# Kernel tuning notes

Measured on AMD Instinct MI355X. Metric: run time of the kernel, lower is better.

## Reference

```python
import jax, jax.numpy as jnp
import numpy as np

N_NODES = 50000
N_EDGES = 800000
D_IN = 96
D_OUT = 96
K_ORDER = 3


def setup_inputs() -> dict:
    key = jax.random.key(0)
    k1, k2, k3, k4, k5 = jax.random.split(key, 5)
    rows = jax.random.randint(k1, (N_EDGES,), 0, N_NODES, dtype=jnp.int64 if jax.config.jax_enable_x64 else jnp.int32)
    cols = jax.random.randint(k2, (N_EDGES,), 0, N_NODES, dtype=jnp.int64 if jax.config.jax_enable_x64 else jnp.int32)
    vals = jax.random.uniform(k3, (N_EDGES,), dtype=jnp.float32) * (1.0 / 16.0)  # ~sym-normalized weights
    H = jax.random.normal(k4, (N_NODES, D_IN), dtype=jnp.float32)
    W = jax.random.normal(k5, (D_IN, D_OUT), dtype=jnp.float32) * (1.0 / np.sqrt(D_IN))
    bias = jnp.zeros((D_OUT,), dtype=jnp.float32)
    return {"rows": rows, "cols": cols, "vals": vals, "H": H, "W": W, "bias": bias}


def reference(rows, cols, vals, H, W, bias):
    n = H.shape[0]

    def spmm(X):  # L @ X via gather-multiply-scatter over COO edges
        return jax.ops.segment_sum(vals[:, None] * X[cols], rows, num_segments=n)

    def ln_mm(X):  # (2L - I) @ X
        return 2.0 * spmm(X) - X

    # k = 0 term: T_0 = H
    H_out = H @ W
    # k = 1 term: T_1 = (2L - I) H  (differentiable, as in torch code)
    T_prev = H
    T_curr = ln_mm(H)
    H_out = H_out + T_curr @ W
    # k >= 2: recurrence computed under no_grad in the original -> stop_gradient
    for _ in range(2, K_ORDER + 1):
        T_next = jax.lax.stop_gradient(2.0 * ln_mm(T_curr) - T_prev)
        H_out = H_out + T_next @ W
        T_prev, T_curr = T_curr, T_next
    return H_out + bias
```

## Files before the change

### kernel.cpp

```cpp
#include <hip/hip_runtime.h>
#include <hip/hip_fp16.h>

#define NN 50000
#define NE 800000
#define D  96
#define NB_SCAN 196
#define N4 (NN * D / 4)
#define CB4 ((N4 + 255) / 256)
#define WFRAG_BLKS 5
#define EMAX (NE + 8 * NN)
#define EZ4  (EMAX / 4)
#define EZB  ((EZ4 + 255) / 256)

typedef unsigned int   uint32;
typedef unsigned short uint16;
typedef short  v8s __attribute__((ext_vector_type(8)));
typedef float  v4f __attribute__((ext_vector_type(4)));
typedef unsigned int v2u __attribute__((ext_vector_type(2)));
typedef unsigned int v4u __attribute__((ext_vector_type(4)));
typedef float v2f __attribute__((ext_vector_type(2)));

__device__ inline uint16 f32_to_bf16(float f) {
    uint32 u = __float_as_uint(f);
    u += 0x7FFF + ((u >> 16) & 1);
    return (uint16)(u >> 16);
}

__device__ inline void u2f(v2u u, float& a, float& b, float& c, float& d) {
    a = __uint_as_float(u.x << 16);
    b = __uint_as_float(u.x & 0xFFFF0000u);
    c = __uint_as_float(u.y << 16);
    d = __uint_as_float(u.y & 0xFFFF0000u);
}

__device__ inline float f16_val(uint32 e) {
    __half_raw h; h.x = (uint16)(e >> 16);
    return __half2float(__half(h));
}

__global__ void prep(const float4* __restrict__ H, ushort4* __restrict__ Hb,
                     const float* __restrict__ W, uint16* __restrict__ Wfrag,
                     int* __restrict__ counts, v4u* __restrict__ edges4) {
    int b = blockIdx.x;
    int t = threadIdx.x;
    if (b < CB4) {
        int i = b * 256 + t;
        if (i < N4) {
            float4 v = H[i];
            ushort4 o;
            o.x = f32_to_bf16(v.x); o.y = f32_to_bf16(v.y);
            o.z = f32_to_bf16(v.z); o.w = f32_to_bf16(v.w);
            Hb[i] = o;
        }
    } else if (b < CB4 + NB_SCAN) {
        int i = (b - CB4) * 256 + t;
        if (i < NN) counts[i] = 0;
    } else if (b < CB4 + NB_SCAN + WFRAG_BLKS) {
        int idx = (b - CB4 - NB_SCAN) * 256 + t;
        if (idx < 18 * 64) {
            int bt = idx >> 6, lane = idx & 63;
            int nt = bt / 3, kc = bt % 3;
            int col = nt * 16 + (lane & 15);
            int kbase = kc * 32 + (lane >> 4) * 8;
            uint16 tmp[8];
            #pragma unroll
            for (int j = 0; j < 8; ++j) tmp[j] = f32_to_bf16(W[(kbase + j) * D + col]);
            uint32* dst = (uint32*)(Wfrag + ((size_t)bt * 64 + lane) * 8);
            const uint32* src = (const uint32*)tmp;
            #pragma unroll
            for (int j = 0; j < 4; ++j) dst[j] = src[j];
        }
    } else {
        int i = (b - CB4 - NB_SCAN - WFRAG_BLKS) * 256 + t;
        if (i < EZ4) edges4[i] = (v4u){0u, 0u, 0u, 0u};
    }
}

__global__ void hist_slots(const int* __restrict__ rows, int* __restrict__ counts,
                           int* __restrict__ slot) {
    int base = (blockIdx.x * blockDim.x + threadIdx.x) * 2;
    if (base < NE) {
        v2u rr = *(const v2u*)(rows + base);
        slot[base]     = atomicAdd(&counts[rr.x], 1);
        slot[base + 1] = atomicAdd(&counts[rr.y], 1);
    }
}

__global__ void scan_p1(const int* __restrict__ counts, int* __restrict__ partials) {
    __shared__ int red[256];
    int t = threadIdx.x;
    int i = blockIdx.x * 256 + t;
    red[t] = (i < NN) ? ((counts[i] + 7) & ~7) : 0;
    __syncthreads();
    for (int off = 128; off > 0; off >>= 1) {
        if (t < off) red[t] += red[t + off];
        __syncthreads();
    }
    if (t == 0) partials[blockIdx.x] = red[0];
}

__global__ void scan_p23(const int* __restrict__ counts, const int* __restrict__ partials,
                         int* __restrict__ row_ptr) {
    __shared__ int pp[256];
    __shared__ int sh[256];
    int t = threadIdx.x;
    pp[t] = (t < NB_SCAN) ? partials[t] : 0;
    __syncthreads();
    for (int off = 1; off < 256; off <<= 1) {
        int u = (t >= off) ? pp[t - off] : 0;
        __syncthreads();
        pp[t] += u;
        __syncthreads();
    }
    int blk_off = (blockIdx.x == 0) ? 0 : pp[blockIdx.x - 1];
    int i = blockIdx.x * 256 + t;
    int v = (i < NN) ? ((counts[i] + 7) & ~7) : 0;
    sh[t] = v;
    __syncthreads();
    for (int off = 1; off < 256; off <<= 1) {
        int u = (t >= off) ? sh[t - off] : 0;
        __syncthreads();
        sh[t] += u;
        __syncthreads();
    }
    int excl = sh[t] - v + blk_off;
    if (i < NN) row_ptr[i] = excl;
    if (i == NN - 1) row_ptr[NN] = excl + v;
}

__global__ void fill_edges(const int* __restrict__ rows, const int* __restrict__ cols,
                           const float* __restrict__ vals, const int* __restrict__ row_ptr,
                           const int* __restrict__ slot, uint32* __restrict__ edges) {
    int base = (blockIdx.x * blockDim.x + threadIdx.x) * 2;
    if (base < NE) {
        v2u rr = *(const v2u*)(rows + base);
        v2u cc = *(const v2u*)(cols + base);
        v2f vv = *(const v2f*)(vals + base);
        v2u ss = *(const v2u*)(slot + base);
        __half_raw h0 = __half_raw(__float2half(vv.x));
        __half_raw h1 = __half_raw(__float2half(vv.y));
        edges[row_ptr[rr.x] + ss.x] = (cc.x & 0xFFFF) | ((uint32)h0.x << 16);
        edges[row_ptr[rr.y] + ss.y] = (cc.y & 0xFFFF) | ((uint32)h1.x << 16);
    }
}

__global__ void spmm(const int* __restrict__ row_ptr, const uint32* __restrict__ edges,
                     const uint16* __restrict__ Xb, uint16* __restrict__ Yb) {
    int tid  = threadIdx.x;
    int lane = tid & 31;
    int g    = tid >> 5;
    int r = blockIdx.x * 8 + g;
    if (r >= NN) return;
    if (lane >= 24) return;

    const v2u* xbase = (const v2u*)Xb;

    float ax = 0.f, ay = 0.f, az = 0.f, aw = 0.f;
    int s = row_ptr[r];
    int e = row_ptr[r + 1];
    int i = s;
    for (; i + 15 < e; i += 16) {
        v4u e0 = *(const v4u*)(edges + i);
        v4u e1 = *(const v4u*)(edges + i + 4);
        v4u e2 = *(const v4u*)(edges + i + 8);
        v4u e3 = *(const v4u*)(edges + i + 12);
        uint32 ee[16] = {e0.x,e0.y,e0.z,e0.w, e1.x,e1.y,e1.z,e1.w,
                         e2.x,e2.y,e2.z,e2.w, e3.x,e3.y,e3.z,e3.w};
        v2u xx[16];
        #pragma unroll
        for (int j = 0; j < 16; ++j)
            xx[j] = xbase[(size_t)(ee[j] & 0xFFFF) * 24 + lane];
        #pragma unroll
        for (int j = 0; j < 16; ++j) {
            float v = f16_val(ee[j]);
            float x0,x1,x2,x3;
            u2f(xx[j], x0,x1,x2,x3);
            ax += v*x0; ay += v*x1; az += v*x2; aw += v*x3;
        }
    }
    for (; i < e; i += 8) {
        v4u ea = *(const v4u*)(edges + i);
        v4u eb = *(const v4u*)(edges + i + 4);
        uint32 ee[8] = {ea.x, ea.y, ea.z, ea.w, eb.x, eb.y, eb.z, eb.w};
        v2u xx[8];
        #pragma unroll
        for (int j = 0; j < 8; ++j)
            xx[j] = xbase[(size_t)(ee[j] & 0xFFFF) * 24 + lane];
        #pragma unroll
        for (int j = 0; j < 8; ++j) {
            float v = f16_val(ee[j]);
            float x0,x1,x2,x3;
            u2f(xx[j], x0,x1,x2,x3);
            ax += v*x0; ay += v*x1; az += v*x2; aw += v*x3;
        }
    }

    v2u o;
    o.x = (uint32)f32_to_bf16(ax) | ((uint32)f32_to_bf16(ay) << 16);
    o.y = (uint32)f32_to_bf16(az) | ((uint32)f32_to_bf16(aw) << 16);
    __builtin_nontemporal_store(o, (v2u*)(Yb + (size_t)r * D) + lane);
}

__global__ void spmm_fuse(const int* __restrict__ row_ptr, const uint32* __restrict__ edges,
                          const uint16* __restrict__ U1, const uint16* __restrict__ U2,
                          uint16* __restrict__ Sb) {
    int tid  = threadIdx.x;
    int lane = tid & 31;
    int g    = tid >> 5;
    int r = blockIdx.x * 8 + g;
    if (r >= NN) return;
    if (lane >= 24) return;

    const v2u* xbase = (const v2u*)U2;

    float ax = 0.f, ay = 0.f, az = 0.f, aw = 0.f;
    int s = row_ptr[r];
    int e = row_ptr[r + 1];
    int i = s;
    for (; i + 15 < e; i += 16) {
        v4u e0 = *(const v4u*)(edges + i);
        v4u e1 = *(const v4u*)(edges + i + 4);
        v4u e2 = *(const v4u*)(edges + i + 8);
        v4u e3 = *(const v4u*)(edges + i + 12);
        uint32 ee[16] = {e0.x,e0.y,e0.z,e0.w, e1.x,e1.y,e1.z,e1.w,
                         e2.x,e2.y,e2.z,e2.w, e3.x,e3.y,e3.z,e3.w};
        v2u xx[16];
        #pragma unroll
        for (int j = 0; j < 16; ++j)
            xx[j] = xbase[(size_t)(ee[j] & 0xFFFF) * 24 + lane];
        #pragma unroll
        for (int j = 0; j < 16; ++j) {
            float v = f16_val(ee[j]);
            float x0,x1,x2,x3;
            u2f(xx[j], x0,x1,x2,x3);
            ax += v*x0; ay += v*x1; az += v*x2; aw += v*x3;
        }
    }
    for (; i < e; i += 8) {
        v4u ea = *(const v4u*)(edges + i);
        v4u eb = *(const v4u*)(edges + i + 4);
        uint32 ee[8] = {ea.x, ea.y, ea.z, ea.w, eb.x, eb.y, eb.z, eb.w};
        v2u xx[8];
        #pragma unroll
        for (int j = 0; j < 8; ++j)
            xx[j] = xbase[(size_t)(ee[j] & 0xFFFF) * 24 + lane];
        #pragma unroll
        for (int j = 0; j < 8; ++j) {
            float v = f16_val(ee[j]);
            float x0,x1,x2,x3;
            u2f(xx[j], x0,x1,x2,x3);
            ax += v*x0; ay += v*x1; az += v*x2; aw += v*x3;
        }
    }

    v2u u1 = __builtin_nontemporal_load((const v2u*)(U1 + (size_t)r * D) + lane);
    v2u u2 = xbase[(size_t)r * 24 + lane];
    float p0,p1,p2,p3, q0,q1,q2,q3;
    u2f(u1, p0,p1,p2,p3);
    u2f(u2, q0,q1,q2,q3);
    float s0 = 12.f*p0 - 40.f*q0 + 32.f*ax;
    float s1 = 12.f*p1 - 40.f*q1 + 32.f*ay;
    float s2 = 12.f*p2 - 40.f*q2 + 32.f*az;
    float s3 = 12.f*p3 - 40.f*q3 + 32.f*aw;

    v2u o;
    o.x = (uint32)f32_to_bf16(s0) | ((uint32)f32_to_bf16(s1) << 16);
    o.y = (uint32)f32_to_bf16(s2) | ((uint32)f32_to_bf16(s3) << 16);
    __builtin_nontemporal_store(o, (v2u*)(Sb + (size_t)r * D) + lane);
}

__global__ void mfma_gemm(const uint16* __restrict__ Sb, const uint16* __restrict__ Wfrag,
                          const float* __restrict__ bias, float* __restrict__ out) {
    int tid   = threadIdx.x;
    int lane  = tid & 63;
    int wv    = blockIdx.x * (blockDim.x >> 6) + (tid >> 6);
    int nwv   = gridDim.x * (blockDim.x >> 6);
    int col   = lane & 15;
    int quad  = lane >> 4;

    v8s wf[6][3];
    #pragma unroll
    for (int nt = 0; nt < 6; ++nt)
        #pragma unroll
        for (int kc = 0; kc < 3; ++kc)
            wf[nt][kc] = ((const v8s*)Wfrag)[(nt * 3 + kc) * 64 + lane];

    float bi[6];
    #pragma unroll
    for (int nt = 0; nt < 6; ++nt) bi[nt] = bias[nt * 16 + col];

    for (int s = wv; s < NN / 16; s += nwv) {
        int r0 = s * 16;
        const uint16* arow = Sb + (size_t)(r0 + col) * D + quad * 8;
        v8s a0 = *((const v8s*)(arow));
        v8s a1 = *((const v8s*)(arow + 32));
        v8s a2 = *((const v8s*)(arow + 64));
        v4f acc[6];
        #pragma unroll
        for (int nt = 0; nt < 6; ++nt) {
            v4f c = {0.f, 0.f, 0.f, 0.f};
            c = __builtin_amdgcn_mfma_f32_16x16x32_bf16(a0, wf[nt][0], c, 0, 0, 0);
            c = __builtin_amdgcn_mfma_f32_16x16x32_bf16(a1, wf[nt][1], c, 0, 0, 0);
            c = __builtin_amdgcn_mfma_f32_16x16x32_bf16(a2, wf[nt][2], c, 0, 0, 0);
            acc[nt] = c;
        }
        #pragma unroll
        for (int nt = 0; nt < 6; ++nt) {
            float* o = out + (size_t)(r0 + quad * 4) * D + nt * 16 + col;
            __builtin_nontemporal_store(acc[nt][0] + bi[nt], o + 0 * D);
            __builtin_nontemporal_store(acc[nt][1] + bi[nt], o + 1 * D);
            __builtin_nontemporal_store(acc[nt][2] + bi[nt], o + 2 * D);
            __builtin_nontemporal_store(acc[nt][3] + bi[nt], o + 3 * D);
        }
    }
}

extern "C" void kernel_launch(void* const* d_in, const int* in_sizes, int n_in,
                              void* d_out, int out_size, void* d_ws, size_t ws_size,
                              hipStream_t stream) {
    const int*   rows = (const int*)d_in[0];
    const int*   cols = (const int*)d_in[1];
    const float* vals = (const float*)d_in[2];
    const float* H    = (const float*)d_in[3];
    const float* W    = (const float*)d_in[4];
    const float* bias = (const float*)d_in[5];
    float* out = (float*)d_out;

    char* ws = (char*)d_ws;
    uint16* Hb       = (uint16*)ws;  ws += (size_t)NN * D * 2;
    uint16* U1b      = (uint16*)ws;  ws += (size_t)NN * D * 2;
    uint16* U2b      = (uint16*)ws;  ws += (size_t)NN * D * 2;
    uint16* Sb       = (uint16*)ws;  ws += (size_t)NN * D * 2;
    uint32* edges    = (uint32*)ws;  ws += (size_t)EMAX * 4;
    uint16* Wfrag    = (uint16*)ws;  ws += (size_t)18 * 64 * 8 * 2;
    int*    counts   = (int*)ws;     ws += (size_t)NN * 4;
    int*    row_ptr  = (int*)ws;     ws += (size_t)(NN + 1) * 4;
    int*    partials = (int*)ws;     ws += 256 * 4;
    int*    slot     = (int*)U2b;

    const int eb2 = (NE / 2 + 255) / 256;

    prep<<<CB4 + NB_SCAN + WFRAG_BLKS + EZB, 256, 0, stream>>>(
        (const float4*)H, (ushort4*)Hb, W, Wfrag, counts, (v4u*)edges);
    hist_slots<<<eb2, 256, 0, stream>>>(rows, counts, slot);
    scan_p1<<<NB_SCAN, 256, 0, stream>>>(counts, partials);
    scan_p23<<<NB_SCAN, 256, 0, stream>>>(counts, partials, row_ptr);
    fill_edges<<<eb2, 256, 0, stream>>>(rows, cols, vals, row_ptr, slot, edges);

    const int sb = (NN + 7) / 8;

    spmm<<<sb, 256, 0, stream>>>(row_ptr, edges, Hb,  U1b);
    spmm<<<sb, 256, 0, stream>>>(row_ptr, edges, U1b, U2b);
    spmm_fuse<<<sb, 256, 0, stream>>>(row_ptr, edges, U1b, U2b, Sb);
    mfma_gemm<<<782, 256, 0, stream>>>(Sb, Wfrag, bias, out);
}
```

Before: 226.4 us.

## Split SpMM feature dimension into three 32-wide blocks with 16-lane row groups

```diff
diff --git a/kernel.cpp b/kernel.cpp
--- a/kernel.cpp
+++ b/kernel.cpp
@@ -11,6 +11,8 @@
 #define EMAX (NE + 8 * NN)
 #define EZ4  (EMAX / 4)
 #define EZB  ((EZ4 + 255) / 256)
+#define RB   3128
+#define NFB  3
 
 typedef unsigned int   uint32;
 typedef unsigned short uint16;
@@ -26,11 +28,9 @@
     return (uint16)(u >> 16);
 }
 
-__device__ inline void u2f(v2u u, float& a, float& b, float& c, float& d) {
-    a = __uint_as_float(u.x << 16);
-    b = __uint_as_float(u.x & 0xFFFF0000u);
-    c = __uint_as_float(u.y << 16);
-    d = __uint_as_float(u.y & 0xFFFF0000u);
+__device__ inline void u1f(uint32 u, float& a, float& b) {
+    a = __uint_as_float(u << 16);
+    b = __uint_as_float(u & 0xFFFF0000u);
 }
 
 __device__ inline float f16_val(uint32 e) {
@@ -147,15 +147,17 @@
 __global__ void spmm(const int* __restrict__ row_ptr, const uint32* __restrict__ edges,
                      const uint16* __restrict__ Xb, uint16* __restrict__ Yb) {
     int tid  = threadIdx.x;
-    int lane = tid & 31;
-    int g    = tid >> 5;
-    int r = blockIdx.x * 8 + g;
+    int lane = tid & 15;
+    int g    = tid >> 4;
+    int bid  = blockIdx.x;
+    int fb   = bid / RB;
+    int rb   = bid - fb * RB;
+    int r    = rb * 16 + g;
     if (r >= NN) return;
-    if (lane >= 24) return;
-
-    const v2u* xbase = (const v2u*)Xb;
-
-    float ax = 0.f, ay = 0.f, az = 0.f, aw = 0.f;
+
+    const uint32* xbase = (const uint32*)(Xb + fb * 32) + lane;
+
+    float a0 = 0.f, a1 = 0.f;
     int s = row_ptr[r];
     int e = row_ptr[r + 1];
     int i = s;
@@ -166,54 +168,54 @@
         v4u e3 = *(const v4u*)(edges + i + 12);
         uint32 ee[16] = {e0.x,e0.y,e0.z,e0.w, e1.x,e1.y,e1.z,e1.w,
                          e2.x,e2.y,e2.z,e2.w, e3.x,e3.y,e3.z,e3.w};
-        v2u xx[16];
+        uint32 xx[16];
         #pragma unroll
         for (int j = 0; j < 16; ++j)
-            xx[j] = xbase[(size_t)(ee[j] & 0xFFFF) * 24 + lane];
+            xx[j] = xbase[(size_t)(ee[j] & 0xFFFF) * 48];
         #pragma unroll
         for (int j = 0; j < 16; ++j) {
             float v = f16_val(ee[j]);
-            float x0,x1,x2,x3;
-            u2f(xx[j], x0,x1,x2,x3);
-            ax += v*x0; ay += v*x1; az += v*x2; aw += v*x3;
+            float x0, x1;
+            u1f(xx[j], x0, x1);
+            a0 += v * x0; a1 += v * x1;
         }
     }
     for (; i < e; i += 8) {
         v4u ea = *(const v4u*)(edges + i);
         v4u eb = *(const v4u*)(edges + i + 4);
         uint32 ee[8] = {ea.x, ea.y, ea.z, ea.w, eb.x, eb.y, eb.z, eb.w};
-        v2u xx[8];
+        uint32 xx[8];
         #pragma unroll
         for (int j = 0; j < 8; ++j)
-            xx[j] = xbase[(size_t)(ee[j] & 0xFFFF) * 24 + lane];
+            xx[j] = xbase[(size_t)(ee[j] & 0xFFFF) * 48];
         #pragma unroll
         for (int j = 0; j < 8; ++j) {
             float v = f16_val(ee[j]);
-            float x0,x1,x2,x3;
-            u2f(xx[j], x0,x1,x2,x3);
-            ax += v*x0; ay += v*x1; az += v*x2; aw += v*x3;
-        }
-    }
-
-    v2u o;
-    o.x = (uint32)f32_to_bf16(ax) | ((uint32)f32_to_bf16(ay) << 16);
-    o.y = (uint32)f32_to_bf16(az) | ((uint32)f32_to_bf16(aw) << 16);
-    __builtin_nontemporal_store(o, (v2u*)(Yb + (size_t)r * D) + lane);
+            float x0, x1;
+            u1f(xx[j], x0, x1);
+            a0 += v * x0; a1 += v * x1;
+        }
+    }
+
+    uint32 o = (uint32)f32_to_bf16(a0) | ((uint32)f32_to_bf16(a1) << 16);
+    __builtin_nontemporal_store(o, (uint32*)Yb + (size_t)r * 48 + fb * 16 + lane);
 }
 
 __global__ void spmm_fuse(const int* __restrict__ row_ptr, const uint32* __restrict__ edges,
                           const uint16* __restrict__ U1, const uint16* __restrict__ U2,
                           uint16* __restrict__ Sb) {
     int tid  = threadIdx.x;
-    int lane = tid & 31;
-    int g    = tid >> 5;
-    int r = blockIdx.x * 8 + g;
+    int lane = tid & 15;
+    int g    = tid >> 4;
+    int bid  = blockIdx.x;
+    int fb   = bid / RB;
+    int rb   = bid - fb * RB;
+    int r    = rb * 16 + g;
     if (r >= NN) return;
-    if (lane >= 24) return;
-
-    const v2u* xbase = (const v2u*)U2;
-
-    float ax = 0.f, ay = 0.f, az = 0.f, aw = 0.f;
+
+    const uint32* xbase = (const uint32*)(U2 + fb * 32) + lane;
+
+    float a0 = 0.f, a1 = 0.f;
     int s = row_ptr[r];
     int e = row_ptr[r + 1];
     int i = s;
@@ -224,49 +226,45 @@
         v4u e3 = *(const v4u*)(edges + i + 12);
         uint32 ee[16] = {e0.x,e0.y,e0.z,e0.w, e1.x,e1.y,e1.z,e1.w,
                          e2.x,e2.y,e2.z,e2.w, e3.x,e3.y,e3.z,e3.w};
-        v2u xx[16];
+        uint32 xx[16];
         #pragma unroll
         for (int j = 0; j < 16; ++j)
-            xx[j] = xbase[(size_t)(ee[j] & 0xFFFF) * 24 + lane];
+            xx[j] = xbase[(size_t)(ee[j] & 0xFFFF) * 48];
         #pragma unroll
         for (int j = 0; j < 16; ++j) {
             float v = f16_val(ee[j]);
-            float x0,x1,x2,x3;
-            u2f(xx[j], x0,x1,x2,x3);
-            ax += v*x0; ay += v*x1; az += v*x2; aw += v*x3;
+            float x0, x1;
+            u1f(xx[j], x0, x1);
+            a0 += v * x0; a1 += v * x1;
         }
     }
     for (; i < e; i += 8) {
         v4u ea = *(const v4u*)(edges + i);
         v4u eb = *(const v4u*)(edges + i + 4);
         uint32 ee[8] = {ea.x, ea.y, ea.z, ea.w, eb.x, eb.y, eb.z, eb.w};
-        v2u xx[8];
+        uint32 xx[8];
         #pragma unroll
         for (int j = 0; j < 8; ++j)
-            xx[j] = xbase[(size_t)(ee[j] & 0xFFFF) * 24 + lane];
+            xx[j] = xbase[(size_t)(ee[j] & 0xFFFF) * 48];
         #pragma unroll
         for (int j = 0; j < 8; ++j) {
             float v = f16_val(ee[j]);
-            float x0,x1,x2,x3;
-            u2f(xx[j], x0,x1,x2,x3);
-            ax += v*x0; ay += v*x1; az += v*x2; aw += v*x3;
-        }
-    }
-
-    v2u u1 = __builtin_nontemporal_load((const v2u*)(U1 + (size_t)r * D) + lane);
-    v2u u2 = xbase[(size_t)r * 24 + lane];
-    float p0,p1,p2,p3, q0,q1,q2,q3;
-    u2f(u1, p0,p1,p2,p3);
-    u2f(u2, q0,q1,q2,q3);
-    float s0 = 12.f*p0 - 40.f*q0 + 32.f*ax;
-    float s1 = 12.f*p1 - 40.f*q1 + 32.f*ay;
-    float s2 = 12.f*p2 - 40.f*q2 + 32.f*az;
-    float s3 = 12.f*p3 - 40.f*q3 + 32.f*aw;
-
-    v2u o;
-    o.x = (uint32)f32_to_bf16(s0) | ((uint32)f32_to_bf16(s1) << 16);
-    o.y = (uint32)f32_to_bf16(s2) | ((uint32)f32_to_bf16(s3) << 16);
-    __builtin_nontemporal_store(o, (v2u*)(Sb + (size_t)r * D) + lane);
+            float x0, x1;
+            u1f(xx[j], x0, x1);
+            a0 += v * x0; a1 += v * x1;
+        }
+    }
+
+    uint32 w1 = ((const uint32*)U1)[(size_t)r * 48 + fb * 16 + lane];
+    uint32 w2 = xbase[(size_t)r * 48];
+    float p0, p1, q0, q1;
+    u1f(w1, p0, p1);
+    u1f(w2, q0, q1);
+    float s0 = 12.f*p0 - 40.f*q0 + 32.f*a0;
+    float s1 = 12.f*p1 - 40.f*q1 + 32.f*a1;
+
+    uint32 o = (uint32)f32_to_bf16(s0) | ((uint32)f32_to_bf16(s1) << 16);
+    __builtin_nontemporal_store(o, (uint32*)Sb + (size_t)r * 48 + fb * 16 + lane);
 }
 
 __global__ void mfma_gemm(const uint16* __restrict__ Sb, const uint16* __restrict__ Wfrag,
@@ -347,10 +345,8 @@
     scan_p23<<<NB_SCAN, 256, 0, stream>>>(counts, partials, row_ptr);
     fill_edges<<<eb2, 256, 0, stream>>>(rows, cols, vals, row_ptr, slot, edges);
 
-    const int sb = (NN + 7) / 8;
-
-    spmm<<<sb, 256, 0, stream>>>(row_ptr, edges, Hb,  U1b);
-    spmm<<<sb, 256, 0, stream>>>(row_ptr, edges, U1b, U2b);
-    spmm_fuse<<<sb, 256, 0, stream>>>(row_ptr, edges, U1b, U2b, Sb);
+    spmm<<<NFB * RB, 256, 0, stream>>>(row_ptr, edges, Hb,  U1b);
+    spmm<<<NFB * RB, 256, 0, stream>>>(row_ptr, edges, U1b, U2b);
+    spmm_fuse<<<NFB * RB, 256, 0, stream>>>(row_ptr, edges, U1b, U2b, Sb);
     mfma_gemm<<<782, 256, 0, stream>>>(Sb, Wfrag, bias, out);
 }
```

Result: slower. 234.6 us (+3.6%).
